# Optimization experiments

Measured on AMD Instinct MI355X. Metric: run time of the kernel, lower is better.

Reference implementation:

```python
import jax, jax.numpy as jnp
import numpy as np

N = 100000
E = 1600000
IN_C, HID_C, OUT_C = 128, 128, 64


def setup_inputs() -> dict:
    key = jax.random.key(0)
    k1, k2, k3, k4, k5, k6 = jax.random.split(key, 6)
    x = jax.random.normal(k1, (N, IN_C), dtype=jnp.float32)
    edge_index = jax.random.randint(k2, (2, E), 0, N, dtype=jnp.int64)
    # Glorot-style init like PyG GCNConv Linear
    W1 = jax.random.normal(k3, (IN_C, HID_C), dtype=jnp.float32) / np.sqrt(IN_C)
    b1 = jnp.zeros((HID_C,), dtype=jnp.float32)
    W2 = jax.random.normal(k4, (HID_C, OUT_C), dtype=jnp.float32) / np.sqrt(HID_C)
    b2 = jnp.zeros((OUT_C,), dtype=jnp.float32)
    return {"x": x, "edge_index": edge_index, "W1": W1, "b1": b1, "W2": W2, "b2": b2}


def gcn_conv(x, src, dst, norm, W, b, n_nodes):
    # x: [N, F_in]; src/dst/norm: [E+N] (self-loops included)
    h = x @ W                                   # [N, F_out] small GEMM
    msg = h[src] * norm[:, None]                # [E+N, F_out] gather (dominant)
    out = jax.ops.segment_sum(msg, dst, num_segments=n_nodes)  # scatter-add
    return out + b


def gcn_norm(edge_index, n_nodes):
    # add self-loops, then symmetric normalization D^-1/2 (A+I) D^-1/2
    loop = jnp.arange(n_nodes, dtype=edge_index.dtype)
    src = jnp.concatenate([edge_index[0], loop])
    dst = jnp.concatenate([edge_index[1], loop])
    deg = jax.ops.segment_sum(jnp.ones_like(dst, dtype=jnp.float32), dst,
                              num_segments=n_nodes)
    dinv = jnp.where(deg > 0, jax.lax.rsqrt(jnp.maximum(deg, 1.0)), 0.0)
    norm = dinv[src] * dinv[dst]
    return src, dst, norm


def reference(x, edge_index, W1, b1, W2, b2):
    n_nodes = x.shape[0]
    src, dst, norm = gcn_norm(edge_index, n_nodes)  # cached=True -> computed once
    h = gcn_conv(x, src, dst, norm, W1, b1, n_nodes)
    h = jax.nn.relu(h)
    # dropout in eval mode (training=False) is identity
    out = gcn_conv(h, src, dst, norm, W2, b2, n_nodes)
    return out
```

## Files before the change

kernel.cpp:

```cpp
#include <hip/hip_runtime.h>
#include <hip/hip_fp16.h>

constexpr int NN  = 100000;
constexpr int NE  = 1600000;
constexpr int TOT = NE + NN;

constexpr int NBUK    = (NN + 255) / 256;
constexpr int EBLOCKS = 512;
constexpr int EPB     = NE / EBLOCKS;

typedef _Float16 f16x8 __attribute__((ext_vector_type(8)));
typedef float    f32x4 __attribute__((ext_vector_type(4)));

__device__ inline float2 h2f2(unsigned int u) {
  __half2 h = __builtin_bit_cast(__half2, u);
  return __half22float2(h);
}
__device__ inline unsigned int f2h2(float a, float b) {
  __half2 h = __floats2half2_rn(a, b);
  return __builtin_bit_cast(unsigned int, h);
}

__global__ __launch_bounds__(256) void k_detect(const unsigned int* __restrict__ ei, int* __restrict__ flag) {
  __shared__ int nz;
  if (threadIdx.x == 0) nz = 0;
  __syncthreads();
  if (ei[threadIdx.x * 2 + 1] != 0u) atomicAdd(&nz, 1);
  __syncthreads();
  if (threadIdx.x == 0) flag[0] = (nz == 0) ? 1 : 0;
}

__device__ inline int load_idx(const void* ei, long long i, int is64) {
  return is64 ? (int)((const long long*)ei)[i] : ((const int*)ei)[i];
}


__global__ __launch_bounds__(256) void k_hist(const void* __restrict__ ei, const int* __restrict__ flag,
                                              int* __restrict__ hist_g) {
  __shared__ int h[NBUK];
  int is64 = flag[0];
  for (int i = threadIdx.x; i < NBUK; i += 256) h[i] = 0;
  __syncthreads();
  int e0 = blockIdx.x * EPB;
  for (int e = e0 + threadIdx.x; e < e0 + EPB; e += 256) {
    int d = load_idx(ei, (long long)NE + e, is64);
    atomicAdd(&h[d >> 8], 1);
  }
  __syncthreads();
  for (int i = threadIdx.x; i < NBUK; i += 256)
    hist_g[i * EBLOCKS + blockIdx.x] = h[i];
}

__global__ __launch_bounds__(512) void k_scan_hist(int* __restrict__ hist_g, int* __restrict__ bucket_total) {
  __shared__ int s[EBLOCKS];
  int b = blockIdx.x, t = threadIdx.x;
  int v = hist_g[b * EBLOCKS + t];
  s[t] = v;
  __syncthreads();
  for (int off = 1; off < EBLOCKS; off <<= 1) {
    int u = (t >= off) ? s[t - off] : 0;
    __syncthreads();
    s[t] += u;
    __syncthreads();
  }
  hist_g[b * EBLOCKS + t] = s[t] - v;
  if (t == EBLOCKS - 1) bucket_total[b] = s[t];
}

__global__ __launch_bounds__(512) void k_scan_buckets(const int* __restrict__ bucket_total,
                                                      int* __restrict__ edge_base, int* __restrict__ row_start) {
  __shared__ int s[512];
  int t = threadIdx.x;
  int v = (t < NBUK) ? bucket_total[t] : 0;
  s[t] = v;
  __syncthreads();
  for (int off = 1; off < 512; off <<= 1) {
    int u = (t >= off) ? s[t - off] : 0;
    __syncthreads();
    s[t] += u;
    __syncthreads();
  }
  if (t <= NBUK) edge_base[t] = s[t] - v;
  if (t == 0) row_start[NN] = TOT;
}

__global__ __launch_bounds__(256) void k_scatter(const void* __restrict__ ei, const int* __restrict__ flag,
                                                 const int* __restrict__ hist_g, const int* __restrict__ edge_base,
                                                 int2* __restrict__ rec) {
  __shared__ int cur[NBUK];
  int is64 = flag[0];
  for (int i = threadIdx.x; i < NBUK; i += 256)
    cur[i] = edge_base[i] + hist_g[i * EBLOCKS + blockIdx.x];
  __syncthreads();
  int e0 = blockIdx.x * EPB;
  for (int e = e0 + threadIdx.x; e < e0 + EPB; e += 256) {
    int sA = load_idx(ei, e, is64);
    int d  = load_idx(ei, (long long)NE + e, is64);
    int p = atomicAdd(&cur[d >> 8], 1);
    rec[p] = make_int2(sA, d);
  }
}

__global__ __launch_bounds__(256) void k_bucket_csr(const int2* __restrict__ rec, const int* __restrict__ edge_base,
                                                    int* __restrict__ row_start, float* __restrict__ dinv,
                                                    int* __restrict__ csr_src) {
  __shared__ int cnt[256];
  __shared__ int s[256];
  int b = blockIdx.x, t = threadIdx.x;
  int node = b * 256 + t;
  cnt[t] = 0;
  __syncthreads();
  int j0 = edge_base[b], j1 = edge_base[b + 1];
  for (int j = j0 + t; j < j1; j += 256)
    atomicAdd(&cnt[rec[j].y & 255], 1);
  __syncthreads();
  int c = (node < NN) ? cnt[t] + 1 : 0;
  s[t] = c;
  __syncthreads();
  for (int off = 1; off < 256; off <<= 1) {
    int u = (t >= off) ? s[t - off] : 0;
    __syncthreads();
    s[t] += u;
    __syncthreads();
  }
  int csr_b = j0 + b * 256;
  int start = csr_b + s[t] - c;
  if (node < NN) {
    row_start[node] = start;
    dinv[node] = rsqrtf((float)c);
    csr_src[start] = node;
  }
  __syncthreads();
  cnt[t] = start + 1;
  __syncthreads();
  for (int j = j0 + t; j < j1; j += 256) {
    int2 r = rec[j];
    int p = atomicAdd(&cnt[r.y & 255], 1);
    csr_src[p] = r.x;
  }
}

template<int OUTC, bool IN_H>
__global__ __launch_bounds__(256) void k_gemm_mfma(const void* __restrict__ Xv,
                                                   const float* __restrict__ W,
                                                   const float* __restrict__ dinv,
                                                   unsigned short* __restrict__ Y) {
  constexpr int NT = OUTC / 16;
  constexpr int PS = 136;
  constexpr int SS = OUTC + 8;
  constexpr int WT_H = OUTC * PS;
  constexpr int ST_H = 64 * SS;
  constexpr int SM_H = WT_H > ST_H ? WT_H : ST_H;
  __shared__ _Float16 smem[SM_H];

  const int tid  = threadIdx.x;
  const int lane = tid & 63;
  const int wv   = tid >> 6;
  const int row0 = blockIdx.x * 64;
  const int l15  = lane & 15;
  const int kg   = lane >> 4;

  for (int idx = tid * 4; idx < 128 * OUTC; idx += 1024) {
    float4 v = *(const float4*)&W[idx];
    int k = idx / OUTC, c = idx % OUTC;
    smem[(c + 0) * PS + k] = (_Float16)v.x;
    smem[(c + 1) * PS + k] = (_Float16)v.y;
    smem[(c + 2) * PS + k] = (_Float16)v.z;
    smem[(c + 3) * PS + k] = (_Float16)v.w;
  }
  __syncthreads();

  int arow = row0 + wv * 16 + l15;
  int rr_g = arow < NN ? arow : NN - 1;

  f32x4 acc[NT];
  #pragma unroll
  for (int n = 0; n < NT; n++) acc[n] = (f32x4){0.f, 0.f, 0.f, 0.f};

  #pragma unroll
  for (int kb = 0; kb < 4; kb++) {
    int k0 = kb * 32 + kg * 8;
    f16x8 a;
    if constexpr (IN_H) {
      a = *(const f16x8*)((const _Float16*)Xv + (size_t)rr_g * 128 + k0);
    } else {
      const float* X = (const float*)Xv;
      float4 v0 = *(const float4*)&X[(size_t)rr_g * 128 + k0];
      float4 v1 = *(const float4*)&X[(size_t)rr_g * 128 + k0 + 4];
      a[0] = (_Float16)v0.x; a[1] = (_Float16)v0.y; a[2] = (_Float16)v0.z; a[3] = (_Float16)v0.w;
      a[4] = (_Float16)v1.x; a[5] = (_Float16)v1.y; a[6] = (_Float16)v1.z; a[7] = (_Float16)v1.w;
    }
    #pragma unroll
    for (int n = 0; n < NT; n++) {
      f16x8 b = *(const f16x8*)&smem[(n * 16 + l15) * PS + k0];
      acc[n] = __builtin_amdgcn_mfma_f32_16x16x32_f16(a, b, acc[n], 0, 0, 0);
    }
  }
  __syncthreads();

  int rb = wv * 16 + kg * 4;
  float dv[4];
  #pragma unroll
  for (int q = 0; q < 4; q++) {
    int gr = row0 + rb + q;
    dv[q] = dinv[gr < NN ? gr : NN - 1];
  }
  #pragma unroll
  for (int n = 0; n < NT; n++)
    #pragma unroll
    for (int q = 0; q < 4; q++)
      smem[(rb + q) * SS + n * 16 + l15] = (_Float16)(acc[n][q] * dv[q]);
  __syncthreads();

  constexpr int SEGS = OUTC / 8;
  for (int u = tid; u < 64 * SEGS; u += 256) {
    int rr = u / SEGS, sg = u % SEGS;
    int gr = row0 + rr;
    if (gr < NN) {
      uint4 v = *(const uint4*)&smem[rr * SS + sg * 8];
      *(uint4*)&Y[(size_t)gr * OUTC + sg * 8] = v;
    }
  }
}

template<int F, bool RELU, bool OUT_H>
__global__ __launch_bounds__(256) void k_agg(const unsigned short* __restrict__ h, const float* __restrict__ dinv,
                                             const int* __restrict__ row_start, const int* __restrict__ csr_src,
                                             const float* __restrict__ bias, void* __restrict__ outv) {
  constexpr int LPN = F / 8;
  constexpr int NPB = 256 / LPN;
  int node = blockIdx.x * NPB + threadIdx.x / LPN;
  int lane = threadIdx.x % LPN;
  if (node >= NN) return;
  int j0 = row_start[node], j1 = row_start[node + 1];
  float acc[8] = {};
  #pragma unroll 2
  for (int j = j0; j < j1; j++) {
    int s = csr_src[j];
    uint4 v = *(const uint4*)&h[(size_t)s * F + lane * 8];
    float2 f;
    f = h2f2(v.x); acc[0] += f.x; acc[1] += f.y;
    f = h2f2(v.y); acc[2] += f.x; acc[3] += f.y;
    f = h2f2(v.z); acc[4] += f.x; acc[5] += f.y;
    f = h2f2(v.w); acc[6] += f.x; acc[7] += f.y;
  }
  float dn = dinv[node];
  float o[8];
  #pragma unroll
  for (int t = 0; t < 8; t++) {
    o[t] = fmaf(dn, acc[t], bias[lane * 8 + t]);
    if (RELU) o[t] = fmaxf(o[t], 0.f);
  }
  if constexpr (OUT_H) {
    unsigned short* out = (unsigned short*)outv;
    uint4 w;
    w.x = f2h2(o[0], o[1]);
    w.y = f2h2(o[2], o[3]);
    w.z = f2h2(o[4], o[5]);
    w.w = f2h2(o[6], o[7]);
    *(uint4*)&out[(size_t)node * F + lane * 8] = w;
  } else {
    float* out = (float*)outv;
    *(float4*)&out[(size_t)node * F + lane * 8]     = make_float4(o[0], o[1], o[2], o[3]);
    *(float4*)&out[(size_t)node * F + lane * 8 + 4] = make_float4(o[4], o[5], o[6], o[7]);
  }
}

extern "C" void kernel_launch(void* const* d_in, const int* in_sizes, int n_in,
                              void* d_out, int out_size, void* d_ws, size_t ws_size,
                              hipStream_t stream) {
  const float* x  = (const float*)d_in[0];
  const void*  ei = d_in[1];
  const float* W1 = (const float*)d_in[2];
  const float* b1 = (const float*)d_in[3];
  const float* W2 = (const float*)d_in[4];
  const float* b2 = (const float*)d_in[5];
  float* out = (float*)d_out;

  char* ws = (char*)d_ws;
  size_t off = 0;
  auto wsalloc = [&](size_t bytes) -> void* {
    void* p = ws + off;
    off += (bytes + 255) & ~(size_t)255;
    return p;
  };
  int*            row_start    = (int*)   wsalloc((NN + 1) * sizeof(int));
  int*            hist_g       = (int*)   wsalloc((size_t)NBUK * EBLOCKS * sizeof(int));
  int*            bucket_total = (int*)   wsalloc(NBUK * sizeof(int));
  int*            edge_base    = (int*)   wsalloc((NBUK + 1) * sizeof(int));
  float*          dinv         = (float*) wsalloc(NN * sizeof(float));
  int*            flag         = (int*)   wsalloc(64);
  int2*           rec          = (int2*)  wsalloc((size_t)NE * sizeof(int2));
  int*            csr_src      = (int*)   wsalloc((size_t)TOT * sizeof(int));
  unsigned short* h1           = (unsigned short*)wsalloc((size_t)NN * 128 * sizeof(unsigned short));
  unsigned short* hmid         = (unsigned short*)wsalloc((size_t)NN * 128 * sizeof(unsigned short));
  unsigned short* hL2          = h1;

  k_detect<<<1, 256, 0, stream>>>((const unsigned int*)ei, flag);
  k_hist<<<EBLOCKS, 256, 0, stream>>>(ei, flag, hist_g);
  k_scan_hist<<<NBUK, EBLOCKS, 0, stream>>>(hist_g, bucket_total);
  k_scan_buckets<<<1, 512, 0, stream>>>(bucket_total, edge_base, row_start);
  k_scatter<<<EBLOCKS, 256, 0, stream>>>(ei, flag, hist_g, edge_base, rec);
  k_bucket_csr<<<NBUK, 256, 0, stream>>>(rec, edge_base, row_start, dinv, csr_src);

  constexpr int GBLK = (NN + 63) / 64;
  k_gemm_mfma<128, false><<<GBLK, 256, 0, stream>>>(x, W1, dinv, h1);
  k_agg<128, true, true><<<(NN + 15) / 16, 256, 0, stream>>>(h1, dinv, row_start, csr_src, b1, hmid);
  k_gemm_mfma<64, true><<<GBLK, 256, 0, stream>>>(hmid, W2, dinv, hL2);
  k_agg<64, false, false><<<(NN + 31) / 32, 256, 0, stream>>>(hL2, dinv, row_start, csr_src, b2, out);
}
```

Baseline: 291.5 us.

## Fuse layer-1 aggregation with layer-2 GEMM and compact edge records

Fuses the first aggregation (bias, ReLU) with the second-layer MFMA GEMM. Each block aggregates 16 nodes into shared memory and multiplies them by W2 there, so the fp16 hidden activations are never written to or read back from global memory. Edge records are packed into one int (src<<8 | dst&255) instead of int2, halving scatter traffic; this only holds while src fits in 23 bits. The separate detect kernel is dropped, and each block now works out index width itself with __syncthreads_count. Each fused block also re-converts W2 into shared memory, which adds per-block overhead.

```diff
diff --git a/kernel.cpp b/kernel.cpp
--- a/kernel.cpp
+++ b/kernel.cpp
@@ -21,13 +21,10 @@
   return __builtin_bit_cast(unsigned int, h);
 }
 
-__global__ __launch_bounds__(256) void k_detect(const unsigned int* __restrict__ ei, int* __restrict__ flag) {
-  __shared__ int nz;
-  if (threadIdx.x == 0) nz = 0;
-  __syncthreads();
-  if (ei[threadIdx.x * 2 + 1] != 0u) atomicAdd(&nz, 1);
-  __syncthreads();
-  if (threadIdx.x == 0) flag[0] = (nz == 0) ? 1 : 0;
+__device__ inline int block_is64(const unsigned int* ei) {
+  unsigned int w = ei[threadIdx.x * 2 + 1];
+  int nz = __syncthreads_count(w != 0u);
+  return nz == 0;
 }
 
 __device__ inline int load_idx(const void* ei, long long i, int is64) {
@@ -35,10 +32,9 @@
 }
 
 
-__global__ __launch_bounds__(256) void k_hist(const void* __restrict__ ei, const int* __restrict__ flag,
-                                              int* __restrict__ hist_g) {
+__global__ __launch_bounds__(256) void k_hist(const void* __restrict__ ei, int* __restrict__ hist_g) {
   __shared__ int h[NBUK];
-  int is64 = flag[0];
+  int is64 = block_is64((const unsigned int*)ei);
   for (int i = threadIdx.x; i < NBUK; i += 256) h[i] = 0;
   __syncthreads();
   int e0 = blockIdx.x * EPB;
@@ -84,11 +80,11 @@
   if (t == 0) row_start[NN] = TOT;
 }
 
-__global__ __launch_bounds__(256) void k_scatter(const void* __restrict__ ei, const int* __restrict__ flag,
+__global__ __launch_bounds__(256) void k_scatter(const void* __restrict__ ei,
                                                  const int* __restrict__ hist_g, const int* __restrict__ edge_base,
-                                                 int2* __restrict__ rec) {
+                                                 int* __restrict__ rec) {
   __shared__ int cur[NBUK];
-  int is64 = flag[0];
+  int is64 = block_is64((const unsigned int*)ei);
   for (int i = threadIdx.x; i < NBUK; i += 256)
     cur[i] = edge_base[i] + hist_g[i * EBLOCKS + blockIdx.x];
   __syncthreads();
@@ -97,11 +93,11 @@
     int sA = load_idx(ei, e, is64);
     int d  = load_idx(ei, (long long)NE + e, is64);
     int p = atomicAdd(&cur[d >> 8], 1);
-    rec[p] = make_int2(sA, d);
-  }
-}
-
-__global__ __launch_bounds__(256) void k_bucket_csr(const int2* __restrict__ rec, const int* __restrict__ edge_base,
+    rec[p] = (sA << 8) | (d & 255);
+  }
+}
+
+__global__ __launch_bounds__(256) void k_bucket_csr(const int* __restrict__ rec, const int* __restrict__ edge_base,
                                                     int* __restrict__ row_start, float* __restrict__ dinv,
                                                     int* __restrict__ csr_src) {
   __shared__ int cnt[256];
@@ -112,7 +108,7 @@
   __syncthreads();
   int j0 = edge_base[b], j1 = edge_base[b + 1];
   for (int j = j0 + t; j < j1; j += 256)
-    atomicAdd(&cnt[rec[j].y & 255], 1);
+    atomicAdd(&cnt[rec[j] & 255], 1);
   __syncthreads();
   int c = (node < NN) ? cnt[t] + 1 : 0;
   s[t] = c;
@@ -134,14 +130,14 @@
   cnt[t] = start + 1;
   __syncthreads();
   for (int j = j0 + t; j < j1; j += 256) {
-    int2 r = rec[j];
-    int p = atomicAdd(&cnt[r.y & 255], 1);
-    csr_src[p] = r.x;
-  }
-}
-
-template<int OUTC, bool IN_H>
-__global__ __launch_bounds__(256) void k_gemm_mfma(const void* __restrict__ Xv,
+    int r = rec[j];
+    int p = atomicAdd(&cnt[r & 255], 1);
+    csr_src[p] = r >> 8;
+  }
+}
+
+template<int OUTC>
+__global__ __launch_bounds__(256) void k_gemm_mfma(const float* __restrict__ X,
                                                    const float* __restrict__ W,
                                                    const float* __restrict__ dinv,
                                                    unsigned short* __restrict__ Y) {
@@ -181,15 +177,10 @@
   for (int kb = 0; kb < 4; kb++) {
     int k0 = kb * 32 + kg * 8;
     f16x8 a;
-    if constexpr (IN_H) {
-      a = *(const f16x8*)((const _Float16*)Xv + (size_t)rr_g * 128 + k0);
-    } else {
-      const float* X = (const float*)Xv;
-      float4 v0 = *(const float4*)&X[(size_t)rr_g * 128 + k0];
-      float4 v1 = *(const float4*)&X[(size_t)rr_g * 128 + k0 + 4];
-      a[0] = (_Float16)v0.x; a[1] = (_Float16)v0.y; a[2] = (_Float16)v0.z; a[3] = (_Float16)v0.w;
-      a[4] = (_Float16)v1.x; a[5] = (_Float16)v1.y; a[6] = (_Float16)v1.z; a[7] = (_Float16)v1.w;
-    }
+    float4 v0 = *(const float4*)&X[(size_t)rr_g * 128 + k0];
+    float4 v1 = *(const float4*)&X[(size_t)rr_g * 128 + k0 + 4];
+    a[0] = (_Float16)v0.x; a[1] = (_Float16)v0.y; a[2] = (_Float16)v0.z; a[3] = (_Float16)v0.w;
+    a[4] = (_Float16)v1.x; a[5] = (_Float16)v1.y; a[6] = (_Float16)v1.z; a[7] = (_Float16)v1.w;
     #pragma unroll
     for (int n = 0; n < NT; n++) {
       f16x8 b = *(const f16x8*)&smem[(n * 16 + l15) * PS + k0];
@@ -223,13 +214,92 @@
   }
 }
 
-template<int F, bool RELU, bool OUT_H>
-__global__ __launch_bounds__(256) void k_agg(const unsigned short* __restrict__ h, const float* __restrict__ dinv,
-                                             const int* __restrict__ row_start, const int* __restrict__ csr_src,
-                                             const float* __restrict__ bias, void* __restrict__ outv) {
-  constexpr int LPN = F / 8;
-  constexpr int NPB = 256 / LPN;
-  int node = blockIdx.x * NPB + threadIdx.x / LPN;
+__global__ __launch_bounds__(256) void k_agg_gemm(const unsigned short* __restrict__ h,
+                                                  const float* __restrict__ dinv,
+                                                  const int* __restrict__ row_start,
+                                                  const int* __restrict__ csr_src,
+                                                  const float* __restrict__ bias,
+                                                  const float* __restrict__ W,
+                                                  unsigned short* __restrict__ Y) {
+  constexpr int PS = 136;
+  constexpr int AS = 136;
+  constexpr int OS = 72;
+  __shared__ _Float16 Wt[64 * PS];
+  __shared__ _Float16 At[16 * AS];
+
+  const int tid = threadIdx.x;
+
+  for (int idx = tid * 4; idx < 128 * 64; idx += 1024) {
+    float4 v = *(const float4*)&W[idx];
+    int k = idx >> 6, c = idx & 63;
+    Wt[(c + 0) * PS + k] = (_Float16)v.x;
+    Wt[(c + 1) * PS + k] = (_Float16)v.y;
+    Wt[(c + 2) * PS + k] = (_Float16)v.z;
+    Wt[(c + 3) * PS + k] = (_Float16)v.w;
+  }
+
+  const int ln    = tid & 15;
+  const int lnode = tid >> 4;
+  const int node  = blockIdx.x * 16 + lnode;
+
+  int j0 = row_start[node], j1 = row_start[node + 1];
+  float acc[8] = {};
+  #pragma unroll 2
+  for (int j = j0; j < j1; j++) {
+    int s = csr_src[j];
+    uint4 v = *(const uint4*)&h[(size_t)s * 128 + ln * 8];
+    float2 f;
+    f = h2f2(v.x); acc[0] += f.x; acc[1] += f.y;
+    f = h2f2(v.y); acc[2] += f.x; acc[3] += f.y;
+    f = h2f2(v.z); acc[4] += f.x; acc[5] += f.y;
+    f = h2f2(v.w); acc[6] += f.x; acc[7] += f.y;
+  }
+  float dn = dinv[node];
+  #pragma unroll
+  for (int t = 0; t < 8; t++) {
+    float o = fmaf(dn, acc[t], bias[ln * 8 + t]);
+    o = fmaxf(o, 0.f);
+    At[lnode * AS + ln * 8 + t] = (_Float16)o;
+  }
+  __syncthreads();
+
+  const int lane = tid & 63;
+  const int wv   = tid >> 6;
+  const int l15  = lane & 15;
+  const int kg   = lane >> 4;
+  f32x4 dacc = (f32x4){0.f, 0.f, 0.f, 0.f};
+  #pragma unroll
+  for (int kb = 0; kb < 4; kb++) {
+    int k0 = kb * 32 + kg * 8;
+    f16x8 a = *(const f16x8*)&At[l15 * AS + k0];
+    f16x8 b = *(const f16x8*)&Wt[(wv * 16 + l15) * PS + k0];
+    dacc = __builtin_amdgcn_mfma_f32_16x16x32_f16(a, b, dacc, 0, 0, 0);
+  }
+  __syncthreads();
+
+  #pragma unroll
+  for (int q = 0; q < 4; q++) {
+    int lr = kg * 4 + q;
+    float dv = dinv[blockIdx.x * 16 + lr];
+    At[lr * OS + wv * 16 + l15] = (_Float16)(dacc[q] * dv);
+  }
+  __syncthreads();
+
+  for (int u = tid; u < 16 * 8; u += 256) {
+    int rr = u >> 3, sg = u & 7;
+    uint4 v = *(const uint4*)&At[rr * OS + sg * 8];
+    *(uint4*)&Y[(size_t)(blockIdx.x * 16 + rr) * 64 + sg * 8] = v;
+  }
+}
+
+__global__ __launch_bounds__(256) void k_agg_final(const unsigned short* __restrict__ h,
+                                                   const float* __restrict__ dinv,
+                                                   const int* __restrict__ row_start,
+                                                   const int* __restrict__ csr_src,
+                                                   const float* __restrict__ bias,
+                                                   float* __restrict__ out) {
+  constexpr int LPN = 8;
+  int node = blockIdx.x * 32 + threadIdx.x / LPN;
   int lane = threadIdx.x % LPN;
   if (node >= NN) return;
   int j0 = row_start[node], j1 = row_start[node + 1];
@@ -237,7 +307,7 @@
   #pragma unroll 2
   for (int j = j0; j < j1; j++) {
     int s = csr_src[j];
-    uint4 v = *(const uint4*)&h[(size_t)s * F + lane * 8];
+    uint4 v = *(const uint4*)&h[(size_t)s * 64 + lane * 8];
     float2 f;
     f = h2f2(v.x); acc[0] += f.x; acc[1] += f.y;
     f = h2f2(v.y); acc[2] += f.x; acc[3] += f.y;
@@ -247,23 +317,9 @@
   float dn = dinv[node];
   float o[8];
   #pragma unroll
-  for (int t = 0; t < 8; t++) {
-    o[t] = fmaf(dn, acc[t], bias[lane * 8 + t]);
-    if (RELU) o[t] = fmaxf(o[t], 0.f);
-  }
-  if constexpr (OUT_H) {
-    unsigned short* out = (unsigned short*)outv;
-    uint4 w;
-    w.x = f2h2(o[0], o[1]);
-    w.y = f2h2(o[2], o[3]);
-    w.z = f2h2(o[4], o[5]);
-    w.w = f2h2(o[6], o[7]);
-    *(uint4*)&out[(size_t)node * F + lane * 8] = w;
-  } else {
-    float* out = (float*)outv;
-    *(float4*)&out[(size_t)node * F + lane * 8]     = make_float4(o[0], o[1], o[2], o[3]);
-    *(float4*)&out[(size_t)node * F + lane * 8 + 4] = make_float4(o[4], o[5], o[6], o[7]);
-  }
+  for (int t = 0; t < 8; t++) o[t] = fmaf(dn, acc[t], bias[lane * 8 + t]);
+  *(float4*)&out[(size_t)node * 64 + lane * 8]     = make_float4(o[0], o[1], o[2], o[3]);
+  *(float4*)&out[(size_t)node * 64 + lane * 8 + 4] = make_float4(o[4], o[5], o[6], o[7]);
 }
 
 extern "C" void kernel_launch(void* const* d_in, const int* in_sizes, int n_in,
@@ -289,23 +345,18 @@
   int*            bucket_total = (int*)   wsalloc(NBUK * sizeof(int));
   int*            edge_base    = (int*)   wsalloc((NBUK + 1) * sizeof(int));
   float*          dinv         = (float*) wsalloc(NN * sizeof(float));
-  int*            flag         = (int*)   wsalloc(64);
-  int2*           rec          = (int2*)  wsalloc((size_t)NE * sizeof(int2));
+  int*            rec          = (int*)   wsalloc((size_t)NE * sizeof(int));
   int*            csr_src      = (int*)   wsalloc((size_t)TOT * sizeof(int));
   unsigned short* h1           = (unsigned short*)wsalloc((size_t)NN * 128 * sizeof(unsigned short));
-  unsigned short* hmid         = (unsigned short*)wsalloc((size_t)NN * 128 * sizeof(unsigned short));
-  unsigned short* hL2          = h1;
-
-  k_detect<<<1, 256, 0, stream>>>((const unsigned int*)ei, flag);
-  k_hist<<<EBLOCKS, 256, 0, stream>>>(ei, flag, hist_g);
+  unsigned short* hL2          = (unsigned short*)wsalloc((size_t)NN * 64 * sizeof(unsigned short));
+
+  k_hist<<<EBLOCKS, 256, 0, stream>>>(ei, hist_g);
   k_scan_hist<<<NBUK, EBLOCKS, 0, stream>>>(hist_g, bucket_total);
   k_scan_buckets<<<1, 512, 0, stream>>>(bucket_total, edge_base, row_start);
-  k_scatter<<<EBLOCKS, 256, 0, stream>>>(ei, flag, hist_g, edge_base, rec);
+  k_scatter<<<EBLOCKS, 256, 0, stream>>>(ei, hist_g, edge_base, rec);
   k_bucket_csr<<<NBUK, 256, 0, stream>>>(rec, edge_base, row_start, dinv, csr_src);
 
-  constexpr int GBLK = (NN + 63) / 64;
-  k_gemm_mfma<128, false><<<GBLK, 256, 0, stream>>>(x, W1, dinv, h1);
-  k_agg<128, true, true><<<(NN + 15) / 16, 256, 0, stream>>>(h1, dinv, row_start, csr_src, b1, hmid);
-  k_gemm_mfma<64, true><<<GBLK, 256, 0, stream>>>(hmid, W2, dinv, hL2);
-  k_agg<64, false, false><<<(NN + 31) / 32, 256, 0, stream>>>(hL2, dinv, row_start, csr_src, b2, out);
-}
+  k_gemm_mfma<128><<<(NN + 63) / 64, 256, 0, stream>>>(x, W1, dinv, h1);
+  k_agg_gemm<<<NN / 16, 256, 0, stream>>>(h1, dinv, row_start, csr_src, b1, W2, hL2);
+  k_agg_final<<<(NN + 31) / 32, 256, 0, stream>>>(hL2, dinv, row_start, csr_src, b2, out);
+}
```

New measurement: 278.0 us. 1.05x faster.
